# Performance work log

Hardware: AMD Instinct MI355X
Metric: run time of the kernel (lower is better)

The kernel has to match this reference:

```python
import jax, jax.numpy as jnp
import numpy as np

B, LQ, LC, LN, D, H = 4, 1024, 1024, 1024, 1024, 16
HD = D // H
LS_INIT = 1e-4
RES_MAX = 10.0
EPS = 1e-5


def layernorm(x, g, b):
    mu = jnp.mean(x, axis=-1, keepdims=True)
    var = jnp.var(x, axis=-1, keepdims=True)
    return (x - mu) * jax.lax.rsqrt(var + EPS) * g + b


def setup_inputs() -> dict:
    key = jax.random.key(0)
    ks = jax.random.split(key, 12)
    s = 0.02
    return {
        "tight_tokens": jax.random.normal(ks[0], (B, LQ, D), jnp.float32),
        "context_tokens": jax.random.normal(ks[1], (B, LC, D), jnp.float32),
        "neighborhood_tokens": jax.random.normal(ks[2], (B, LN, D), jnp.float32),
        "ln_q_g": jnp.ones((D,), jnp.float32), "ln_q_b": jnp.zeros((D,), jnp.float32),
        "ln_kv_g": jnp.ones((D,), jnp.float32), "ln_kv_b": jnp.zeros((D,), jnp.float32),
        "in_proj_w": jax.random.normal(ks[3], (3 * D, D), jnp.float32) * s,
        "in_proj_b": jnp.zeros((3 * D,), jnp.float32),
        "out_proj_w": jax.random.normal(ks[4], (D, D), jnp.float32) * s,
        "out_proj_b": jnp.zeros((D,), jnp.float32),
        "cross_gamma": jnp.full((D,), LS_INIT, jnp.float32),
        "ln_f_g": jnp.ones((D,), jnp.float32), "ln_f_b": jnp.zeros((D,), jnp.float32),
        "w1": jax.random.normal(ks[5], (4 * D, D), jnp.float32) * s,
        "b1": jnp.zeros((4 * D,), jnp.float32),
        "w2": jax.random.normal(ks[6], (D, 4 * D), jnp.float32) * s,
        "b2": jnp.zeros((D,), jnp.float32),
        "ffn_gamma": jnp.full((D,), LS_INIT, jnp.float32),
    }


def reference(tight_tokens, context_tokens, neighborhood_tokens,
              ln_q_g, ln_q_b, ln_kv_g, ln_kv_b,
              in_proj_w, in_proj_b, out_proj_w, out_proj_b, cross_gamma,
              ln_f_g, ln_f_b, w1, b1, w2, b2, ffn_gamma):
    kv = jnp.concatenate([context_tokens, neighborhood_tokens], axis=1)  # [B, LKV, D]
    q_in = layernorm(tight_tokens, ln_q_g, ln_q_b)
    kv_in = layernorm(kv, ln_kv_g, ln_kv_b)

    wq, wk, wv = jnp.split(in_proj_w, 3, axis=0)
    bq, bk, bv = jnp.split(in_proj_b, 3, axis=0)
    q = (q_in @ wq.T + bq).reshape(B, LQ, H, HD)
    k = (kv_in @ wk.T + bk).reshape(B, -1, H, HD)
    v = (kv_in @ wv.T + bv).reshape(B, -1, H, HD)

    scores = jnp.einsum('bqhd,bkhd->bhqk', q, k) / jnp.sqrt(jnp.float32(HD))
    attn = jax.nn.softmax(scores, axis=-1)  # [B, H, LQ, LKV]
    ctx = jnp.einsum('bhqk,bkhd->bqhd', attn, v).reshape(B, LQ, D)
    attn_out = ctx @ out_proj_w.T + out_proj_b

    cg = jnp.clip(cross_gamma, -RES_MAX, RES_MAX)
    x = tight_tokens + attn_out * cg

    h = layernorm(x, ln_f_g, ln_f_b)
    h = jax.nn.gelu(h @ w1.T + b1, approximate=False) @ w2.T + b2
    fg = jnp.clip(ffn_gamma, -RES_MAX, RES_MAX)
    x = x + h * fg

    return x, attn.mean(axis=1)
```

## Files before the change

### kernel.cpp

```cpp
#include <hip/hip_runtime.h>
#include <math.h>

typedef unsigned short u16;
typedef __attribute__((ext_vector_type(8))) short bf16x8;
typedef __attribute__((ext_vector_type(4))) float f32x4;

#define MFMA16(a,b,c) __builtin_amdgcn_mfma_f32_16x16x32_bf16(a,b,c,0,0,0)

__device__ __forceinline__ u16 f2bf(float f){
  union { float f; unsigned int u; } x; x.f = f;
  unsigned int r = x.u + 0x7fffu + ((x.u >> 16) & 1u);
  return (u16)(r >> 16);
}

__device__ __forceinline__ void gload16(const void* g, void* lds){
  __builtin_amdgcn_global_load_lds(
    (const __attribute__((address_space(1))) unsigned int*)g,
    (__attribute__((address_space(3))) unsigned int*)lds, 16, 0, 0);
}

__global__ __launch_bounds__(256) void cvt_weights(
    const float* __restrict__ wqkv, const float* __restrict__ wo,
    const float* __restrict__ w1, const float* __restrict__ w2,
    u16* __restrict__ o0, u16* __restrict__ o1,
    u16* __restrict__ o2, u16* __restrict__ o3)
{
  int idx = blockIdx.x * 256 + threadIdx.x;
  const float* src; u16* dst;
  if (idx < 786432)                    { src = wqkv; dst = o0; }
  else if ((idx -= 786432) < 262144)   { src = wo;   dst = o1; }
  else if ((idx -= 262144) < 1048576)  { src = w1;   dst = o2; }
  else { idx -= 1048576;                 src = w2;   dst = o3; }
  float4 v = ((const float4*)src)[idx];
  short4 o;
  o.x = (short)f2bf(v.x); o.y = (short)f2bf(v.y);
  o.z = (short)f2bf(v.z); o.w = (short)f2bf(v.w);
  ((short4*)dst)[idx] = o;
}

__device__ __forceinline__ void ln_row(
    const float* src, const float* g, const float* be, u16* out, long orow, int t)
{
  float4 v = ((const float4*)src)[t];
  float s  = v.x + v.y + v.z + v.w;
  float ss = v.x*v.x + v.y*v.y + v.z*v.z + v.w*v.w;
  #pragma unroll
  for (int m = 1; m < 64; m <<= 1) { s += __shfl_xor(s, m); ss += __shfl_xor(ss, m); }
  __shared__ float red[8];
  int l = t & 63, w = t >> 6;
  if (l == 0) { red[w*2] = s; red[w*2+1] = ss; }
  __syncthreads();
  s  = red[0] + red[2] + red[4] + red[6];
  ss = red[1] + red[3] + red[5] + red[7];
  float mean = s * (1.0f/1024.0f);
  float var  = ss * (1.0f/1024.0f) - mean*mean;
  float rstd = rsqrtf(var + 1e-5f);
  float4 gv = ((const float4*)g)[t];
  float4 bv = ((const float4*)be)[t];
  short4 o;
  o.x = (short)f2bf((v.x-mean)*rstd*gv.x + bv.x);
  o.y = (short)f2bf((v.y-mean)*rstd*gv.y + bv.y);
  o.z = (short)f2bf((v.z-mean)*rstd*gv.z + bv.z);
  o.w = (short)f2bf((v.w-mean)*rstd*gv.w + bv.w);
  *(short4*)(out + orow*1024 + t*4) = o;
}

__global__ __launch_bounds__(256) void ln_in(
    const float* __restrict__ tight, const float* __restrict__ ctxt,
    const float* __restrict__ nbh,
    const float* __restrict__ qg, const float* __restrict__ qb,
    const float* __restrict__ kg, const float* __restrict__ kb,
    u16* __restrict__ qout, u16* __restrict__ kvout)
{
  int row = blockIdx.x, t = threadIdx.x;
  if (row < 4096) {
    ln_row(tight + (long)row*1024, qg, qb, qout, row, t);
  } else {
    int r2 = row - 4096;
    int b = r2 >> 11, p = r2 & 2047;
    const float* src = (p < 1024) ? ctxt + ((long)(b*1024 + p))*1024
                                  : nbh + ((long)(b*1024 + p - 1024))*1024;
    ln_row(src, kg, kb, kvout, r2, t);
  }
}

__global__ __launch_bounds__(256) void ln_mid(
    const float* __restrict__ s0,
    const float* __restrict__ g, const float* __restrict__ be,
    u16* __restrict__ out)
{
  int row = blockIdx.x, t = threadIdx.x;
  ln_row(s0 + (long)row*1024, g, be, out, row, t);
}

template<int EPI, int BM>
__global__ __launch_bounds__(256,2) void gemm_bt(
    const u16* __restrict__ A, const u16* __restrict__ Bt,
    int M, int N, int K,
    const float* __restrict__ bias,
    const float* __restrict__ gamma,
    const float* __restrict__ resid,
    float* __restrict__ outf,
    u16* __restrict__ outb0, u16* __restrict__ outb1)
{
  constexpr int MI = BM / 32;
  __shared__ __align__(16) u16 at[2][BM*64];
  __shared__ __align__(16) u16 bt[2][128*64];
  int nwg = gridDim.x;
  int bidx = (blockIdx.x & 7) * (nwg >> 3) + (blockIdx.x >> 3);
  int nb = N >> 7;
  int tm = bidx / nb, tn = bidx % nb;
  int m0 = tm * BM, n0 = tn << 7;
  int t = threadIdx.x, l = t & 63, w = t >> 6;
  int wr = (w >> 1) * (BM/2), wc = (w & 1) * 64;
  int fr = l & 15, fq = l >> 4;
  f32x4 acc[MI][4] = {};
  int rr = t >> 3;
  int cb = (t & 7) << 4;
  const char* Ab = (const char*)A;
  const char* Bp = (const char*)Bt;
  long ld = (long)K * 2;

#define G_STAGE(s, kt) do {                                                        \
    _Pragma("unroll")                                                              \
    for (int c = 0; c < MI; c++) {                                                 \
      int row = c*32 + rr;                                                         \
      gload16(Ab + (long)(m0 + row)*ld + (long)(kt)*2 + (cb ^ ((row & 7) << 4)),   \
              (char*)at[s] + c*4096 + w*1024);                                     \
    }                                                                              \
    _Pragma("unroll")                                                              \
    for (int c = 0; c < 4; c++) {                                                  \
      int row = c*32 + rr;                                                         \
      gload16(Bp + (long)(n0 + row)*ld + (long)(kt)*2 + (cb ^ ((row & 7) << 4)),   \
              (char*)bt[s] + c*4096 + w*1024);                                     \
    }                                                                              \
  } while (0)

  G_STAGE(0, 0);
  __syncthreads();
  int cur = 0;
  for (int kt = 0; kt < K; kt += 64) {
    if (kt + 64 < K) G_STAGE(cur ^ 1, kt + 64);
    #pragma unroll
    for (int ka = 0; ka < 2; ka++) {
      bf16x8 af[MI], bfv[4];
      #pragma unroll
      for (int i = 0; i < MI; i++) {
        int ra = wr + i*16 + fr;
        af[i] = *(const bf16x8*)((const char*)at[cur] + ra*128 + ((ka*64 + fq*16) ^ ((ra & 7) << 4)));
      }
      #pragma unroll
      for (int j = 0; j < 4; j++) {
        int rb = wc + j*16 + fr;
        bfv[j] = *(const bf16x8*)((const char*)bt[cur] + rb*128 + ((ka*64 + fq*16) ^ ((rb & 7) << 4)));
      }
      #pragma unroll
      for (int i = 0; i < MI; i++)
        #pragma unroll
        for (int j = 0; j < 4; j++)
          acc[i][j] = MFMA16(af[i], bfv[j], acc[i][j]);
    }
    __syncthreads();
    cur ^= 1;
  }
#undef G_STAGE
  #pragma unroll
  for (int i = 0; i < MI; i++) {
    #pragma unroll
    for (int j = 0; j < 4; j++) {
      #pragma unroll
      for (int r = 0; r < 4; r++) {
        int row = m0 + wr + i*16 + fq*4 + r;
        int col = n0 + wc + j*16 + fr;
        float v = acc[i][j][r];
        if constexpr (EPI == 0) {
          float qv = (v + bias[col]) * 0.18033688011112042f;
          int b = row >> 10, lq = row & 1023, h = col >> 6, hd = col & 63;
          outb0[(((long)(b*16 + h)) << 16) + (lq << 6) + hd] = f2bf(qv);
        } else if constexpr (EPI == 2) {
          float gs = gamma[col]; gs = fminf(fmaxf(gs, -10.f), 10.f);
          long idx = (long)row*1024 + col;
          outf[idx] = resid[idx] + (v + bias[col]) * gs;
        } else if constexpr (EPI == 3) {
          float u = v + bias[col];
          float ge = 0.5f * u * (1.0f + erff(u * 0.70710678118654752f));
          outb0[(long)row*4096 + col] = f2bf(ge);
        } else {
          float gs = gamma[col]; gs = fminf(fmaxf(gs, -10.f), 10.f);
          long idx = (long)row*1024 + col;
          outf[idx] = resid[idx] + (v + bias[col]) * gs;
        }
      }
    }
  }
}

template<int EPI>
__global__ __launch_bounds__(512, 2) void gemm256(
    const u16* __restrict__ A, const u16* __restrict__ Bt,
    int M, int N, int K,
    const float* __restrict__ bias,
    u16* __restrict__ outb0, u16* __restrict__ outb1)
{
  __shared__ __align__(16) u16 As[2][256*64];
  __shared__ __align__(16) u16 Bs[2][256*64];
  int nwg = gridDim.x;
  int bidx = (blockIdx.x & 7) * (nwg >> 3) + (blockIdx.x >> 3);
  int nb = N >> 8;
  int tm = bidx / nb, tn = bidx % nb;
  int m0 = tm << 8, n0 = tn << 8;
  int t = threadIdx.x, l = t & 63, w = t >> 6;
  int wm = w >> 2, wn = w & 3;
  int fr = l & 15, fq = l >> 4;
  int sr = t >> 3;
  int scb = (t & 7) << 4;
  int s7 = (sr & 7) << 4;
  const char* Ab = (const char*)A;
  const char* Bp = (const char*)Bt;
  long ld = (long)K * 2;

#define STAGE_AQ(slot, kt, q) do {                                               \
    int grow = (sr < 32) ? ((q)*32 + sr) : (128 + (q)*32 + sr - 32);             \
    int abase = (w < 4) ? ((q)*32 + w*8) : (128 + (q)*32 + (w - 4)*8);           \
    gload16(Ab + (long)(m0 + grow)*ld + (long)(kt)*2 + (scb ^ s7),               \
            (char*)As[slot] + abase*128);                                        \
  } while (0)
#define STAGE_BH(slot, kt, h) do {                                               \
    int r0 = (h)*128 + sr;                                                       \
    gload16(Bp + (long)(n0 + r0)*ld + (long)(kt)*2 + (scb ^ s7),                 \
            (char*)Bs[slot] + ((h)*128 + w*8)*128);                              \
    gload16(Bp + (long)(n0 + r0 + 64)*ld + (long)(kt)*2 + (scb ^ s7),            \
            (char*)Bs[slot] + ((h)*128 + 64 + w*8)*128);                         \
  } while (0)

  f32x4 acc[8][4] = {};
  int NT = K >> 6;

  STAGE_BH(0, 0, 0); STAGE_BH(0, 0, 1);
  STAGE_AQ(0, 0, 0); STAGE_AQ(0, 0, 1); STAGE_AQ(0, 0, 2); STAGE_AQ(0, 0, 3);
  STAGE_BH(1, 64, 0); STAGE_BH(1, 64, 1);
  asm volatile("s_waitcnt vmcnt(4)" ::: "memory");
  __builtin_amdgcn_s_barrier();
  asm volatile("" ::: "memory");

#define MFMA_PHASE(mibase)                                                       \
    __builtin_amdgcn_s_setprio(1);                                               \
    _Pragma("unroll")                                                            \
    for (int nj = 0; nj < 4; nj++) {                                             \
      acc[(mibase)][nj]   = MFMA16(a00, bfr[nj][0], acc[(mibase)][nj]);          \
      acc[(mibase)][nj]   = MFMA16(a01, bfr[nj][1], acc[(mibase)][nj]);          \
      acc[(mibase)+1][nj] = MFMA16(a10, bfr[nj][0], acc[(mibase)+1][nj]);        \
      acc[(mibase)+1][nj] = MFMA16(a11, bfr[nj][1], acc[(mibase)+1][nj]);        \
    }                                                                            \
    __builtin_amdgcn_s_setprio(0);

#define READ_A(p)                                                                \
    int r0_ = wm*128 + (2*(p))*16 + fr;                                          \
    int r1_ = r0_ + 16;                                                          \
    bf16x8 a00 = *(const bf16x8*)(Ab_s + r0_*128 + ((fq*16) ^ ((r0_ & 7) << 4)));        \
    bf16x8 a01 = *(const bf16x8*)(Ab_s + r0_*128 + ((64 + fq*16) ^ ((r0_ & 7) << 4)));   \
    bf16x8 a10 = *(const bf16x8*)(Ab_s + r1_*128 + ((fq*16) ^ ((r1_ & 7) << 4)));        \
    bf16x8 a11 = *(const bf16x8*)(Ab_s + r1_*128 + ((64 + fq*16) ^ ((r1_ & 7) << 4)));

  for (int tt = 0; tt < NT; tt++) {
    int s = tt & 1;
    const char* Ab_s = (const char*)As[s];
    const char* Bb_s = (const char*)Bs[s];
    int kt1 = (tt + 1) << 6, kt2 = (tt + 2) << 6;
    bf16x8 bfr[4][2];
    {
      #pragma unroll
      for (int nj = 0; nj < 4; nj++) {
        int rb = wn*64 + nj*16 + fr;
        bfr[nj][0] = *(const bf16x8*)(Bb_s + rb*128 + ((fq*16) ^ ((rb & 7) << 4)));
        bfr[nj][1] = *(const bf16x8*)(Bb_s + rb*128 + ((64 + fq*16) ^ ((rb & 7) << 4)));
      }
      READ_A(0)
      if (tt + 1 < NT) { STAGE_AQ(s ^ 1, kt1, 0); STAGE_AQ(s ^ 1, kt1, 1); }
      asm volatile("s_waitcnt lgkmcnt(8)" ::: "memory");
      __builtin_amdgcn_s_barrier();
      asm volatile("s_waitcnt lgkmcnt(0)" ::: "memory");
      MFMA_PHASE(0)
      __builtin_amdgcn_s_barrier();
    }
    {
      READ_A(1)
      if (tt + 1 < NT) { STAGE_AQ(s ^ 1, kt1, 2); STAGE_AQ(s ^ 1, kt1, 3); }
      __builtin_amdgcn_s_barrier();
      asm volatile("s_waitcnt lgkmcnt(0)" ::: "memory");
      MFMA_PHASE(2)
      __builtin_amdgcn_s_barrier();
    }
    {
      READ_A(2)
      if (tt + 2 < NT) STAGE_BH(s, kt2, 0);
      __builtin_amdgcn_s_barrier();
      asm volatile("s_waitcnt lgkmcnt(0)" ::: "memory");
      MFMA_PHASE(4)
      __builtin_amdgcn_s_barrier();
    }
    {
      READ_A(3)
      if (tt + 2 < NT) STAGE_BH(s, kt2, 1);
      __builtin_amdgcn_s_barrier();
      asm volatile("s_waitcnt lgkmcnt(0)" ::: "memory");
      MFMA_PHASE(6)
      if (tt + 1 < NT) {
        if (tt + 2 < NT) { asm volatile("s_waitcnt vmcnt(4)" ::: "memory"); }
        else             { asm volatile("s_waitcnt vmcnt(0)" ::: "memory"); }
      }
      __builtin_amdgcn_s_barrier();
      asm volatile("" ::: "memory");
    }
  }
#undef READ_A
#undef MFMA_PHASE
#undef STAGE_AQ
#undef STAGE_BH

  #pragma unroll
  for (int mi = 0; mi < 8; mi++) {
    #pragma unroll
    for (int nj = 0; nj < 4; nj++) {
      #pragma unroll
      for (int r = 0; r < 4; r++) {
        int row = m0 + wm*128 + mi*16 + fq*4 + r;
        int col = n0 + wn*64 + nj*16 + fr;
        float v = acc[mi][nj][r];
        if constexpr (EPI == 1) {
          float u = v + bias[col];
          int b = row >> 11, p = row & 2047;
          if (col < 1024) {
            int h = col >> 6, hd = col & 63;
            outb0[(((long)((b*16 + h)*2048 + p)) << 6) + hd] = f2bf(u);
          } else {
            int c2 = col - 1024, h = c2 >> 6, hd = c2 & 63;
            outb1[(((long)((b*16 + h)*64 + hd)) << 11) + p] = f2bf(u);
          }
        } else {
          float u = v + bias[col];
          float ge = 0.5f * u * (1.0f + erff(u * 0.70710678118654752f));
          outb0[(long)row*4096 + col] = f2bf(ge);
        }
      }
    }
  }
}

__global__ __launch_bounds__(256, 3) void flash_fwd(
    const u16* __restrict__ q, const u16* __restrict__ k,
    const u16* __restrict__ vt, u16* __restrict__ ctx,
    float* __restrict__ ilout)
{
  __shared__ __align__(16) u16 ks[2][64*64];
  __shared__ __align__(16) u16 vs[2][64*64];
  __shared__ __align__(16) char ps[4*4096];
  int nwg = gridDim.x;
  int bid = (blockIdx.x & 7) * (nwg >> 3) + (blockIdx.x >> 3);
  int qt = bid & 7, h = (bid >> 3) & 15, b = bid >> 7;
  int q0 = qt << 7;
  int t = threadIdx.x, l = t & 63, w = t >> 6;
  int fr = l & 15, fq = l >> 4;
  const char* qb = (const char*)(q  + (((long)(b*16 + h)) << 16));
  const char* kb = (const char*)(k  + (((long)(b*16 + h)) << 17));
  const char* vb = (const char*)(vt + (((long)(b*16 + h)) << 17));
  char* psw = ps + w*4096;
  int rr = t >> 3;
  int sc = (t & 7) << 4;

  #pragma unroll
  for (int c = 0; c < 2; c++) {
    int row = c*32 + rr;
    gload16(kb + (long)row*128 + (sc ^ ((row & 7) << 4)), (char*)ks[0] + c*4096 + w*1024);
    gload16(vb + (long)row*4096 + (sc ^ ((row & 7) << 4)), (char*)vs[0] + c*4096 + w*1024);
  }
  {
    int qr = l >> 3;
    #pragma unroll
    for (int c = 0; c < 4; c++) {
      int row = c*8 + qr;
      gload16(qb + (long)(q0 + w*32 + row)*128 + (sc ^ ((row & 7) << 4)), psw + c*1024);
    }
  }
  asm volatile("s_waitcnt vmcnt(0)" ::: "memory");
  bf16x8 qf[2][2];
  #pragma unroll
  for (int rf = 0; rf < 2; rf++) {
    int row = rf*16 + fr;
    qf[rf][0] = *(const bf16x8*)(psw + row*128 + ((fq*16) ^ ((row & 7) << 4)));
    qf[rf][1] = *(const bf16x8*)(psw + row*128 + ((64 + fq*16) ^ ((row & 7) << 4)));
  }
  asm volatile("s_waitcnt lgkmcnt(0)" ::: "memory");
  __builtin_amdgcn_s_barrier();
  asm volatile("" ::: "memory");

  f32x4 cacc[2][4] = {};
  f32x4 lrun[2] = {{0.f,0.f,0.f,0.f},{0.f,0.f,0.f,0.f}};
  int cur = 0;
  for (int kt = 0; kt < 2048; kt += 64) {
    int notlast = (kt + 64 < 2048);
    if (notlast) {
      #pragma unroll
      for (int c = 0; c < 2; c++) {
        int row = c*32 + rr;
        gload16(vb + (long)row*4096 + (long)(kt + 64)*2 + (sc ^ ((row & 7) << 4)),
                (char*)vs[cur ^ 1] + c*4096 + w*1024);
        gload16(kb + (long)(kt + 64 + row)*128 + (sc ^ ((row & 7) << 4)),
                (char*)ks[cur ^ 1] + c*4096 + w*1024);
      }
    }
    __builtin_amdgcn_sched_barrier(0);
    const char* ksb = (const char*)ks[cur];
    f32x4 sf[2][4];
    __builtin_amdgcn_s_setprio(1);
    #pragma unroll
    for (int cf = 0; cf < 4; cf++) {
      int row = cf*16 + fr;
      bf16x8 kf0 = *(const bf16x8*)(ksb + row*128 + ((fq*16) ^ ((row & 7) << 4)));
      bf16x8 kf1 = *(const bf16x8*)(ksb + row*128 + ((64 + fq*16) ^ ((row & 7) << 4)));
      #pragma unroll
      for (int rf = 0; rf < 2; rf++) {
        f32x4 a = {};
        a = MFMA16(qf[rf][0], kf0, a);
        sf[rf][cf] = MFMA16(qf[rf][1], kf1, a);
      }
    }
    __builtin_amdgcn_s_setprio(0);
    #pragma unroll
    for (int rf = 0; rf < 2; rf++)
      #pragma unroll
      for (int cf = 0; cf < 4; cf++)
        #pragma unroll
        for (int r = 0; r < 4; r++) {
          float pv = exp2f(sf[rf][cf][r]);
          lrun[rf][r] += pv;
          union { float f; unsigned int u; } pu; pu.f = pv;
          int prow = rf*16 + fq*4 + r;
          *(u16*)(psw + prow*128 + (((cf*16 + fr) << 1) ^ ((prow & 7) << 4))) = (u16)(pu.u >> 16);
        }
    bf16x8 pa[2][2];
    #pragma unroll
    for (int rf = 0; rf < 2; rf++) {
      int row = rf*16 + fr;
      pa[rf][0] = *(const bf16x8*)(psw + row*128 + ((fq*16) ^ ((row & 7) << 4)));
      pa[rf][1] = *(const bf16x8*)(psw + row*128 + ((64 + fq*16) ^ ((row & 7) << 4)));
    }
    __builtin_amdgcn_s_setprio(1);
    #pragma unroll
    for (int cfd = 0; cfd < 4; cfd++) {
      int hd = cfd*16 + fr;
      bf16x8 vf0 = *(const bf16x8*)((const char*)vs[cur] + hd*128 + ((fq*16) ^ ((hd & 7) << 4)));
      bf16x8 vf1 = *(const bf16x8*)((const char*)vs[cur] + hd*128 + ((64 + fq*16) ^ ((hd & 7) << 4)));
      #pragma unroll
      for (int rf = 0; rf < 2; rf++) {
        cacc[rf][cfd] = MFMA16(pa[rf][0], vf0, cacc[rf][cfd]);
        cacc[rf][cfd] = MFMA16(pa[rf][1], vf1, cacc[rf][cfd]);
      }
    }
    __builtin_amdgcn_s_setprio(0);
    if (notlast) {
      asm volatile("s_waitcnt vmcnt(0)" ::: "memory");
      __builtin_amdgcn_s_barrier();
      asm volatile("" ::: "memory");
    }
    cur ^= 1;
  }
  #pragma unroll
  for (int rf = 0; rf < 2; rf++) {
    float il4[4];
    #pragma unroll
    for (int r = 0; r < 4; r++) {
      float s = lrun[rf][r];
      #pragma unroll
      for (int msk = 1; msk < 16; msk <<= 1) s += __shfl_xor(s, msk, 16);
      il4[r] = 1.0f / s;
    }
    #pragma unroll
    for (int cf = 0; cf < 4; cf++)
      #pragma unroll
      for (int r = 0; r < 4; r++) {
        int row = q0 + w*32 + rf*16 + fq*4 + r;
        int col = h*64 + cf*16 + fr;
        ctx[(long)(b*1024 + row)*1024 + col] = f2bf(cacc[rf][cf][r] * il4[r]);
      }
    if (fr == 0) {
      #pragma unroll
      for (int r = 0; r < 4; r++) {
        int row = q0 + w*32 + rf*16 + fq*4 + r;
        long idx = (((long)(b*16 + h)) << 10) + row;
        ilout[idx] = il4[r];
      }
    }
  }
}

__global__ __launch_bounds__(256,2) void attn_mean(
    const u16* __restrict__ q, const u16* __restrict__ k,
    const float* __restrict__ il,
    float* __restrict__ out)
{
  __shared__ __align__(16) u16 qs[2][128*64];
  __shared__ __align__(16) u16 ks[2][128*64];
  __shared__ __align__(16) float ml[2][128];
  int nwg = gridDim.x;
  int bid = (blockIdx.x & 7) * (nwg >> 3) + (blockIdx.x >> 3);
  int kt = bid & 15, qt = (bid >> 4) & 7, b = bid >> 7;
  int q0 = qt << 7, k0 = kt << 7;
  int t = threadIdx.x, l = t & 63, w = t >> 6;
  int wr = (w >> 1) << 6, wc = (w & 1) << 6;
  int fr = l & 15, fq = l >> 4;
  int rr = t >> 3, cbb = (t & 7) << 4;
  const long bh = (long)b * 16;

#define AM_STAGE(hh, s) do {                                                        \
    const char* qb_ = (const char*)(q + ((bh + (hh)) << 16)) + (long)q0*128;        \
    const char* kb_ = (const char*)(k + ((bh + (hh)) << 17)) + (long)k0*128;        \
    _Pragma("unroll")                                                               \
    for (int c = 0; c < 4; c++) {                                                   \
      int row = c*32 + rr;                                                          \
      int sw = cbb ^ ((row & 7) << 4);                                              \
      gload16(qb_ + (long)row*128 + sw, (char*)qs[s] + c*4096 + w*1024);            \
      gload16(kb_ + (long)row*128 + sw, (char*)ks[s] + c*4096 + w*1024);            \
    }                                                                               \
    if (w == 0 && l < 32) {                                                         \
      gload16((const char*)(il + ((bh + (hh)) << 10) + q0) + l*16, (char*)ml[s]);   \
    }                                                                               \
  } while (0)

  AM_STAGE(0, 0);
  asm volatile("s_waitcnt vmcnt(0)" ::: "memory");
  __builtin_amdgcn_s_barrier();
  asm volatile("" ::: "memory");

  f32x4 macc[4][4] = {};
  for (int h = 0; h < 16; h++) {
    int cur = h & 1;
    if (h < 15) AM_STAGE(h + 1, cur ^ 1);
    const char* qsb = (const char*)qs[cur];
    const char* ksb = (const char*)ks[cur];
    const float* mlb = ml[cur];
    f32x4 ir4[4];
    #pragma unroll
    for (int i = 0; i < 4; i++)
      ir4[i] = *(const f32x4*)(mlb + wr + i*16 + fq*4);
    bf16x8 af[4][2], bf[4][2];
    #pragma unroll
    for (int i = 0; i < 4; i++) {
      int ra = wr + i*16 + fr;
      int rb = wc + i*16 + fr;
      af[i][0] = *(const bf16x8*)(qsb + ra*128 + ((fq*16) ^ ((ra & 7) << 4)));
      af[i][1] = *(const bf16x8*)(qsb + ra*128 + ((64 + fq*16) ^ ((ra & 7) << 4)));
      bf[i][0] = *(const bf16x8*)(ksb + rb*128 + ((fq*16) ^ ((rb & 7) << 4)));
      bf[i][1] = *(const bf16x8*)(ksb + rb*128 + ((64 + fq*16) ^ ((rb & 7) << 4)));
    }
    #pragma unroll
    for (int j = 0; j < 4; j++) {
      f32x4 sf[4];
      __builtin_amdgcn_s_setprio(1);
      #pragma unroll
      for (int i = 0; i < 4; i++) {
        f32x4 a = MFMA16(af[i][0], bf[j][0], {});
        sf[i] = MFMA16(af[i][1], bf[j][1], a);
      }
      __builtin_amdgcn_s_setprio(0);
      #pragma unroll
      for (int i = 0; i < 4; i++)
        #pragma unroll
        for (int r = 0; r < 4; r++)
          macc[i][j][r] += exp2f(sf[i][r]) * ir4[i][r];
    }
    asm volatile("s_waitcnt vmcnt(0)" ::: "memory");
    __builtin_amdgcn_s_barrier();
    asm volatile("" ::: "memory");
  }
#undef AM_STAGE
  #pragma unroll
  for (int i = 0; i < 4; i++)
    #pragma unroll
    for (int j = 0; j < 4; j++)
      #pragma unroll
      for (int r = 0; r < 4; r++) {
        int row = q0 + wr + i*16 + fq*4 + r;
        int col = k0 + wc + j*16 + fr;
        out[((long)(b*1024 + row) << 11) + col] = macc[i][j][r] * 0.0625f;
      }
}

extern "C" void kernel_launch(void* const* d_in, const int* in_sizes, int n_in,
                              void* d_out, int out_size, void* d_ws, size_t ws_size,
                              hipStream_t stream)
{
  (void)in_sizes; (void)n_in; (void)out_size; (void)ws_size;
  const float* tight = (const float*)d_in[0];
  const float* ctxt  = (const float*)d_in[1];
  const float* nbh   = (const float*)d_in[2];
  const float* lnqg  = (const float*)d_in[3];
  const float* lnqb  = (const float*)d_in[4];
  const float* lnkg  = (const float*)d_in[5];
  const float* lnkb  = (const float*)d_in[6];
  const float* wqkv  = (const float*)d_in[7];
  const float* bqkv  = (const float*)d_in[8];
  const float* wo    = (const float*)d_in[9];
  const float* bo    = (const float*)d_in[10];
  const float* cg    = (const float*)d_in[11];
  const float* lnfg  = (const float*)d_in[12];
  const float* lnfb  = (const float*)d_in[13];
  const float* w1    = (const float*)d_in[14];
  const float* b1    = (const float*)d_in[15];
  const float* w2    = (const float*)d_in[16];
  const float* b2    = (const float*)d_in[17];
  const float* fg    = (const float*)d_in[18];

  char* p = (char*)d_ws;
  u16* wqkv_bf = (u16*)p; p += 3072L*1024*2;
  u16* wo_bf   = (u16*)p; p += 1024L*1024*2;
  u16* w1_bf   = (u16*)p; p += 4096L*1024*2;
  u16* w2_bf   = (u16*)p; p += 1024L*4096*2;
  u16* qin_bf  = (u16*)p; p += 4096L*1024*2;
  u16* kvin_bf = (u16*)p; p += 8192L*1024*2;
  u16* q_bf    = (u16*)p; p += 4L*16*1024*64*2;
  u16* k_bf    = (u16*)p; p += 4L*16*2048*64*2;
  u16* vt_bf   = (u16*)p; p += 4L*16*64*2048*2;
  u16* ctx_bf  = (u16*)p; p += 4096L*1024*2;
  float* il_f  = (float*)p; p += 4L*16*1024*4;
  float* x_f   = (float*)p; p += 4096L*1024*4;
  u16* hln_bf  = (u16*)p; p += 4096L*1024*2;
  u16* gelu_bf = (u16*)p; p += 4096L*4096*2;

  float* x_out    = (float*)d_out;
  float* mean_out = x_out + 4194304;

  cvt_weights<<<12288, 256, 0, stream>>>(wqkv, wo, w1, w2, wqkv_bf, wo_bf, w1_bf, w2_bf);
  ln_in<<<12288, 256, 0, stream>>>(tight, ctxt, nbh, lnqg, lnqb, lnkg, lnkb,
                                   qin_bf, kvin_bf);
  gemm_bt<0,64><<<512, 256, 0, stream>>>(qin_bf, wqkv_bf, 4096, 1024, 1024,
                                      bqkv, nullptr, nullptr, nullptr, q_bf, nullptr);
  gemm256<1><<<256, 512, 0, stream>>>(kvin_bf, wqkv_bf + 1024L*1024, 8192, 2048, 1024,
                                      bqkv + 1024, k_bf, vt_bf);
  flash_fwd<<<512, 256, 0, stream>>>(q_bf, k_bf, vt_bf, ctx_bf, il_f);
  attn_mean<<<512, 256, 0, stream>>>(q_bf, k_bf, il_f, mean_out);
  gemm_bt<2,64><<<512, 256, 0, stream>>>(ctx_bf, wo_bf, 4096, 1024, 1024,
                                      bo, cg, tight, x_f, nullptr, nullptr);
  ln_mid<<<4096, 256, 0, stream>>>(x_f, lnfg, lnfb, hln_bf);
  gemm256<3><<<256, 512, 0, stream>>>(hln_bf, w1_bf, 4096, 4096, 1024,
                                      b1, gelu_bf, nullptr);
  gemm_bt<4,64><<<512, 256, 0, stream>>>(gelu_bf, w2_bf, 4096, 1024, 4096,
                                      b2, fg, x_f, x_out, nullptr, nullptr);
}
```

Before: 359.3 us.

## Collapse per-phase barriers in GEMM main loop into one barrier per k-tile

The GEMM k-loop used to interleave its async global-to-LDS stages with four MFMA phases, putting a barrier pair around every phase. Now the B fragments are read into registers first, one barrier follows, and all A and B prefetches for the next tiles are issued together. The four A-read/MFMA phases then run back-to-back with no barriers, and a single barrier closes each k-tile. The goal is to cut barrier stalls and keep the matrix units busy, at the cost of bursting all memory traffic at the start of each tile instead of spreading it across phases. The prologue staging order is also swapped so the A tile is issued before B.

```diff
diff --git a/kernel.cpp b/kernel.cpp
--- a/kernel.cpp
+++ b/kernel.cpp
@@ -236,8 +236,8 @@
   f32x4 acc[8][4] = {};
   int NT = K >> 6;
 
+  STAGE_AQ(0, 0, 0); STAGE_AQ(0, 0, 1); STAGE_AQ(0, 0, 2); STAGE_AQ(0, 0, 3);
   STAGE_BH(0, 0, 0); STAGE_BH(0, 0, 1);
-  STAGE_AQ(0, 0, 0); STAGE_AQ(0, 0, 1); STAGE_AQ(0, 0, 2); STAGE_AQ(0, 0, 3);
   STAGE_BH(1, 64, 0); STAGE_BH(1, 64, 1);
   asm volatile("s_waitcnt vmcnt(4)" ::: "memory");
   __builtin_amdgcn_s_barrier();
@@ -268,47 +268,27 @@
     const char* Bb_s = (const char*)Bs[s];
     int kt1 = (tt + 1) << 6, kt2 = (tt + 2) << 6;
     bf16x8 bfr[4][2];
-    {
-      #pragma unroll
-      for (int nj = 0; nj < 4; nj++) {
-        int rb = wn*64 + nj*16 + fr;
-        bfr[nj][0] = *(const bf16x8*)(Bb_s + rb*128 + ((fq*16) ^ ((rb & 7) << 4)));
-        bfr[nj][1] = *(const bf16x8*)(Bb_s + rb*128 + ((64 + fq*16) ^ ((rb & 7) << 4)));
-      }
-      READ_A(0)
-      if (tt + 1 < NT) { STAGE_AQ(s ^ 1, kt1, 0); STAGE_AQ(s ^ 1, kt1, 1); }
-      asm volatile("s_waitcnt lgkmcnt(8)" ::: "memory");
-      __builtin_amdgcn_s_barrier();
-      asm volatile("s_waitcnt lgkmcnt(0)" ::: "memory");
-      MFMA_PHASE(0)
-      __builtin_amdgcn_s_barrier();
-    }
-    {
-      READ_A(1)
-      if (tt + 1 < NT) { STAGE_AQ(s ^ 1, kt1, 2); STAGE_AQ(s ^ 1, kt1, 3); }
-      __builtin_amdgcn_s_barrier();
-      asm volatile("s_waitcnt lgkmcnt(0)" ::: "memory");
-      MFMA_PHASE(2)
-      __builtin_amdgcn_s_barrier();
-    }
-    {
-      READ_A(2)
-      if (tt + 2 < NT) STAGE_BH(s, kt2, 0);
-      __builtin_amdgcn_s_barrier();
-      asm volatile("s_waitcnt lgkmcnt(0)" ::: "memory");
-      MFMA_PHASE(4)
-      __builtin_amdgcn_s_barrier();
-    }
-    {
-      READ_A(3)
-      if (tt + 2 < NT) STAGE_BH(s, kt2, 1);
-      __builtin_amdgcn_s_barrier();
-      asm volatile("s_waitcnt lgkmcnt(0)" ::: "memory");
-      MFMA_PHASE(6)
-      if (tt + 1 < NT) {
-        if (tt + 2 < NT) { asm volatile("s_waitcnt vmcnt(4)" ::: "memory"); }
-        else             { asm volatile("s_waitcnt vmcnt(0)" ::: "memory"); }
-      }
+    #pragma unroll
+    for (int nj = 0; nj < 4; nj++) {
+      int rb = wn*64 + nj*16 + fr;
+      bfr[nj][0] = *(const bf16x8*)(Bb_s + rb*128 + ((fq*16) ^ ((rb & 7) << 4)));
+      bfr[nj][1] = *(const bf16x8*)(Bb_s + rb*128 + ((64 + fq*16) ^ ((rb & 7) << 4)));
+    }
+    asm volatile("s_waitcnt lgkmcnt(0)" ::: "memory");
+    __builtin_amdgcn_s_barrier();
+    asm volatile("" ::: "memory");
+    if (tt + 1 < NT) {
+      STAGE_AQ(s ^ 1, kt1, 0); STAGE_AQ(s ^ 1, kt1, 1);
+      STAGE_AQ(s ^ 1, kt1, 2); STAGE_AQ(s ^ 1, kt1, 3);
+    }
+    if (tt + 2 < NT) { STAGE_BH(s, kt2, 0); STAGE_BH(s, kt2, 1); }
+    { READ_A(0) MFMA_PHASE(0) }
+    { READ_A(1) MFMA_PHASE(2) }
+    { READ_A(2) MFMA_PHASE(4) }
+    { READ_A(3) MFMA_PHASE(6) }
+    if (tt + 1 < NT) {
+      if (tt + 2 < NT) { asm volatile("s_waitcnt vmcnt(4)" ::: "memory"); }
+      else             { asm volatile("s_waitcnt vmcnt(0)" ::: "memory"); }
       __builtin_amdgcn_s_barrier();
       asm volatile("" ::: "memory");
     }
```

After: 368.3 us. 1.03x slower.
